# Kernel optimization log

Hardware: AMD Instinct MI355X
Metric: run time of the kernel (lower is better)

Reference implementation:

```python
import jax, jax.numpy as jnp
import numpy as np

N, E, H, L, G = 50000, 500000, 128, 4, 1000
EPS = 1e-7      # GENConv message eps
LN_EPS = 1e-5   # torch LayerNorm default


def setup_inputs() -> dict:
    key = jax.random.key(0)
    ks = jax.random.split(key, 24)
    d = {}
    d["x"] = jax.random.normal(ks[0], (N, 9), jnp.float32)
    d["edge_index"] = jax.random.randint(ks[1], (2, E), 0, N, jnp.int32)
    d["edge_attr"] = jax.random.normal(ks[2], (E, 3), jnp.float32)
    d["batch"] = jnp.sort(jax.random.randint(ks[3], (N,), 0, G, jnp.int32))
    s9, s3, sh, s2h = 1/np.sqrt(9), 1/np.sqrt(3), 1/np.sqrt(H), 1/np.sqrt(2*H)
    u = lambda k, shp, s: jax.random.uniform(k, shp, jnp.float32, -s, s)
    d["enc_node_W"] = u(ks[4], (9, H), s9)
    d["enc_node_b"] = u(ks[5], (H,), s9)
    d["enc_edge_W"] = u(ks[6], (3, H), s3)
    d["enc_edge_b"] = u(ks[7], (H,), s3)
    d["ln_g"] = jnp.ones((L, H), jnp.float32)   # DeepGCNLayer pre-norm affine
    d["ln_b"] = jnp.zeros((L, H), jnp.float32)
    d["W1"] = u(ks[8], (L, H, 2*H), sh)          # GENConv MLP layer 1
    d["b1"] = u(ks[9], (L, 2*H), sh)
    d["mlp_ln_g"] = jnp.ones((L, 2*H), jnp.float32)
    d["mlp_ln_b"] = jnp.zeros((L, 2*H), jnp.float32)
    d["W2"] = u(ks[10], (L, 2*H, H), s2h)        # GENConv MLP layer 2
    d["b2"] = u(ks[11], (L, H), s2h)
    d["t"] = jnp.ones((L,), jnp.float32)         # learnable softmax temperature, init 1.0
    return d


def layernorm(x, g, b):
    mu = x.mean(-1, keepdims=True)
    var = ((x - mu) ** 2).mean(-1, keepdims=True)
    return (x - mu) / jnp.sqrt(var + LN_EPS) * g + b


def genconv(h, src, dst, ea, t, W1, b1, lg, lb, W2, b2):
    # message: relu(x_j + edge_attr) + eps   -> [E, H]
    msg = jax.nn.relu(h[src] + ea) + EPS
    # softmax aggregation over incoming edges, per channel
    logits = t * msg
    m = jax.ops.segment_max(logits, dst, num_segments=N)
    num = jnp.exp(logits - m[dst])
    den = jax.ops.segment_sum(num, dst, num_segments=N)
    alpha = num / den[dst]
    agg = jax.ops.segment_sum(msg * alpha, dst, num_segments=N)
    out = agg + h  # root residual inside GENConv
    z = jax.nn.relu(layernorm(out @ W1 + b1, lg, lb))
    return z @ W2 + b2


def reference(x, edge_index, edge_attr, batch, enc_node_W, enc_node_b,
              enc_edge_W, enc_edge_b, ln_g, ln_b, W1, b1, mlp_ln_g, mlp_ln_b,
              W2, b2, t):
    src, dst = edge_index[0], edge_index[1]
    h = x @ enc_node_W + enc_node_b            # node encoder  [N, H]
    ea = edge_attr @ enc_edge_W + enc_edge_b   # edge encoder  [E, H]
    # layer 0: conv only (DeeperGCN forward uses layers[0].conv directly)
    h = genconv(h, src, dst, ea, t[0], W1[0], b1[0], mlp_ln_g[0], mlp_ln_b[0], W2[0], b2[0])
    # layers 1..L-1: res+ block: x + conv(relu(LN(x))); dropout is identity (eval)
    for i in range(1, L):
        z = jax.nn.relu(layernorm(h, ln_g[i], ln_b[i]))
        h = h + genconv(z, src, dst, ea, t[i], W1[i], b1[i], mlp_ln_g[i], mlp_ln_b[i], W2[i], b2[i])
    h = jax.nn.relu(layernorm(h, ln_g[0], ln_b[0]))  # reuses layer-0 norm
    # global mean pool over graphs
    counts = jax.ops.segment_sum(jnp.ones((N,), h.dtype), batch, num_segments=G)
    sums = jax.ops.segment_sum(h, batch, num_segments=G)
    return sums / jnp.maximum(counts, 1.0)[:, None]
```

## Files before the change

kernel.cpp:

```cpp
#include <hip/hip_runtime.h>

#define NN 50000
#define NE 500000
#define HD 128
#define HD2 256
#define NL 4
#define NG 1000

constexpr float MSG_EPS = 1e-7f;
constexpr float LNEPS   = 1e-5f;

typedef float  f32x4  __attribute__((ext_vector_type(4)));
typedef __bf16 bf16x8 __attribute__((ext_vector_type(8)));

__device__ __forceinline__ unsigned short f2b(float f) {
    unsigned int u = __float_as_uint(f);
    unsigned int r = u + 0x7FFFu + ((u >> 16) & 1u);
    return (unsigned short)(r >> 16);
}
__device__ __forceinline__ float b2f(unsigned short h) {
    return __uint_as_float(((unsigned int)h) << 16);
}
__device__ __forceinline__ unsigned int pack2(float a, float b) {
    return (unsigned int)f2b(a) | ((unsigned int)f2b(b) << 16);
}

#define PREP_BLKS 512
#define ENC_BLKS 25000
#define HIST_BLKS ((NE + 255) / 256)

__global__ void k_setup(const float* __restrict__ x, const float* __restrict__ encW,
                        const float* __restrict__ encB, unsigned short* __restrict__ zb,
                        const float* __restrict__ W1, const float* __restrict__ W2,
                        unsigned short* __restrict__ W1T, unsigned short* __restrict__ W2T,
                        const int* __restrict__ dst, int* __restrict__ counts) {
    int bid = blockIdx.x, tid = threadIdx.x;
    if (bid < PREP_BLKS) {
        int idx = bid * 256 + tid;
        {
            int k = idx & 127, n = (idx >> 7) & 255, l = idx >> 15;
            W1T[idx] = f2b(W1[(l * 128 + k) * 256 + n]);
        }
        {
            int k = idx & 255, n = (idx >> 8) & 127, l = idx >> 15;
            W2T[idx] = f2b(W2[(l * 256 + k) * 128 + n]);
        }
    } else if (bid < PREP_BLKS + ENC_BLKS) {
        int n = (bid - PREP_BLKS) * 2 + (tid >> 7);
        int c = tid & 127;
        float xr[9];
#pragma unroll
        for (int k = 0; k < 9; k++) xr[k] = x[n * 9 + k];
        float acc = encB[c];
#pragma unroll
        for (int k = 0; k < 9; k++) acc = fmaf(xr[k], encW[k * HD + c], acc);
        zb[(size_t)n * HD + c] = f2b(acc);
    } else {
        int e = (bid - PREP_BLKS - ENC_BLKS) * 256 + tid;
        if (e < NE) atomicAdd(&counts[dst[e]], 1);
    }
}

#define SCAN_B 512
#define NSB ((NN + SCAN_B - 1) / SCAN_B)

__global__ void k_scan1(const int* __restrict__ counts, int* __restrict__ incl,
                        int* __restrict__ bsum) {
    __shared__ int s[SCAN_B];
    int i = blockIdx.x * SCAN_B + threadIdx.x;
    int v = (i < NN) ? counts[i] : 0;
    s[threadIdx.x] = v;
    __syncthreads();
    for (int off = 1; off < SCAN_B; off <<= 1) {
        int t = (threadIdx.x >= off) ? s[threadIdx.x - off] : 0;
        __syncthreads();
        s[threadIdx.x] += t;
        __syncthreads();
    }
    if (i < NN) incl[i] = s[threadIdx.x];
    if (threadIdx.x == SCAN_B - 1) bsum[blockIdx.x] = s[threadIdx.x];
}

__global__ void k_scan2(const int* __restrict__ bsum, int* __restrict__ boff, int nb) {
    __shared__ int s[128];
    int v = (threadIdx.x < nb) ? bsum[threadIdx.x] : 0;
    s[threadIdx.x] = v;
    __syncthreads();
    for (int off = 1; off < 128; off <<= 1) {
        int t = (threadIdx.x >= off) ? s[threadIdx.x - off] : 0;
        __syncthreads();
        s[threadIdx.x] += t;
        __syncthreads();
    }
    if (threadIdx.x < nb) boff[threadIdx.x] = s[threadIdx.x] - v;
}

__global__ void k_scan3g(const int* __restrict__ incl, const int* __restrict__ boff,
                         int* __restrict__ row_start, const int* __restrict__ batch,
                         int* __restrict__ gstart) {
    if (blockIdx.x < NSB) {
        int i = blockIdx.x * SCAN_B + threadIdx.x;
        if (i < NN) row_start[i + 1] = incl[i] + boff[blockIdx.x];
        if (i == 0) row_start[0] = 0;
    } else {
        int g = (blockIdx.x - NSB) * SCAN_B + threadIdx.x;
        if (g > NG) return;
        int lo = 0, hi = NN;
        while (lo < hi) {
            int mid = (lo + hi) >> 1;
            if (batch[mid] < g) lo = mid + 1;
            else hi = mid;
        }
        gstart[g] = lo;
    }
}

__global__ void k_scatter(const int* __restrict__ src, const int* __restrict__ dst,
                          const float* __restrict__ eattr, const int* __restrict__ row_start,
                          int* __restrict__ cursor, float4* __restrict__ aperm) {
    int e = blockIdx.x * blockDim.x + threadIdx.x;
    if (e >= NE) return;
    int d = dst[e];
    int p = row_start[d] + atomicAdd(&cursor[d], 1);
    float4 v;
    v.x = eattr[e * 3 + 0];
    v.y = eattr[e * 3 + 1];
    v.z = eattr[e * 3 + 2];
    v.w = __int_as_float(src[e]);
    aperm[p] = v;
}

__device__ __forceinline__ void edge_acc2(float4 a, unsigned int zz, float2 w0, float2 w1,
                                          float2 w2, float2 bb, float tv, float& num0,
                                          float& num1, float& wm0, float& wm1) {
    float zx = b2f((unsigned short)zz), zy = b2f((unsigned short)(zz >> 16));
    float eax = fmaf(a.x, w0.x, fmaf(a.y, w1.x, fmaf(a.z, w2.x, bb.x)));
    float eay = fmaf(a.x, w0.y, fmaf(a.y, w1.y, fmaf(a.z, w2.y, bb.y)));
    float mx = fmaxf(zx + eax, 0.f) + MSG_EPS;
    float my = fmaxf(zy + eay, 0.f) + MSG_EPS;
    float ex = __expf(tv * mx), ey = __expf(tv * my);
    num0 += ex;
    num1 += ey;
    wm0 = fmaf(mx, ex, wm0);
    wm1 = fmaf(my, ey, wm1);
}

__global__ __launch_bounds__(256) void k_aggregate(const unsigned short* __restrict__ zbin,
                                                   const float4* __restrict__ aperm,
                                                   const int* __restrict__ row_start,
                                                   const float* __restrict__ We,
                                                   const float* __restrict__ be,
                                                   const float* __restrict__ t, int layer,
                                                   unsigned int* __restrict__ outb) {
    __shared__ float4 part[4][64];
    int w = threadIdx.x >> 6, lane = threadIdx.x & 63;
    int n = blockIdx.x * 2 + (w >> 1);
    int half = w & 1;
    int c = lane * 2;
    float2 w0 = *(const float2*)&We[c];
    float2 w1 = *(const float2*)&We[HD + c];
    float2 w2 = *(const float2*)&We[2 * HD + c];
    float2 bb = *(const float2*)&be[c];
    float tv = t[layer];
    int s0 = row_start[n], s1 = row_start[n + 1];
    int mid = s0 + ((s1 - s0 + 1) >> 1);
    int lo = half ? mid : s0;
    int hi = half ? s1 : mid;
    float num0 = 0.f, num1 = 0.f, wm0 = 0.f, wm1 = 0.f;
    const unsigned int* z32 = (const unsigned int*)zbin;
    int p = lo;
    for (; p + 4 <= hi; p += 4) {
        float4 A[4];
#pragma unroll
        for (int j = 0; j < 4; j++) A[j] = aperm[p + j];
        unsigned int Z[4];
#pragma unroll
        for (int j = 0; j < 4; j++) {
            int sj = __builtin_amdgcn_readfirstlane(__float_as_int(A[j].w));
            Z[j] = z32[(size_t)sj * 64 + lane];
        }
#pragma unroll
        for (int j = 0; j < 4; j++)
            edge_acc2(A[j], Z[j], w0, w1, w2, bb, tv, num0, num1, wm0, wm1);
    }
    for (; p < hi; p++) {
        float4 a = aperm[p];
        int sj = __builtin_amdgcn_readfirstlane(__float_as_int(a.w));
        unsigned int zz = z32[(size_t)sj * 64 + lane];
        edge_acc2(a, zz, w0, w1, w2, bb, tv, num0, num1, wm0, wm1);
    }
    part[w][lane] = make_float4(num0, num1, wm0, wm1);
    __syncthreads();
    if (half == 0) {
        float4 a = part[w][lane];
        float4 b = part[w + 1][lane];
        float n0 = a.x + b.x, n1 = a.y + b.y;
        float m0 = a.z + b.z, m1 = a.w + b.w;
        unsigned int zn = z32[(size_t)n * 64 + lane];
        bool has = s1 > s0;
        float ox = (has ? (m0 / n0) : 0.f) + b2f((unsigned short)zn);
        float oy = (has ? (m1 / n1) : 0.f) + b2f((unsigned short)(zn >> 16));
        outb[(size_t)n * 64 + lane] = pack2(ox, oy);
    }
}

#define BM 32
#define HS_LD 264
#define HT_LD 136

__global__ __launch_bounds__(256) void k_mlp(const unsigned short* __restrict__ outb,
                                             const unsigned short* __restrict__ W1T,
                                             const float* __restrict__ b1l,
                                             const float* __restrict__ lgl,
                                             const float* __restrict__ lbl,
                                             const unsigned short* __restrict__ W2T,
                                             const float* __restrict__ b2l,
                                             unsigned short* __restrict__ h,
                                             const float* __restrict__ gn,
                                             const float* __restrict__ bn,
                                             unsigned short* __restrict__ zb,
                                             int add_residual) {
    __shared__ __align__(16) unsigned short Hs[BM * HS_LD];
    __shared__ __align__(16) unsigned short Ht[BM * HT_LD];
    __shared__ __align__(16) float2 st1[2][16][4];

    int nb = blockIdx.x * BM;
    int tid = threadIdx.x;
    int w = tid >> 6, lane = tid & 63, q = lane >> 4, i = lane & 15;

    f32x4 acc[2][4];
#pragma unroll
    for (int rt = 0; rt < 2; rt++)
#pragma unroll
        for (int ct = 0; ct < 4; ct++) acc[rt][ct] = (f32x4){0.f, 0.f, 0.f, 0.f};

    bf16x8 acur[2], bcur[4];
#pragma unroll
    for (int rt = 0; rt < 2; rt++) {
        int row = nb + rt * 16 + i;
        acur[rt] = (row < NN) ? *(const bf16x8*)&outb[(size_t)row * HD + q * 8]
                              : (bf16x8)(__bf16)0.f;
    }
#pragma unroll
    for (int ct = 0; ct < 4; ct++)
        bcur[ct] = *(const bf16x8*)&W1T[(w * 64 + ct * 16 + i) * HD + q * 8];

#pragma unroll
    for (int ks = 0; ks < 4; ks++) {
        bf16x8 anxt[2], bnxt[4];
        if (ks < 3) {
#pragma unroll
            for (int rt = 0; rt < 2; rt++) {
                int row = nb + rt * 16 + i;
                anxt[rt] = (row < NN)
                               ? *(const bf16x8*)&outb[(size_t)row * HD + (ks + 1) * 32 + q * 8]
                               : (bf16x8)(__bf16)0.f;
            }
#pragma unroll
            for (int ct = 0; ct < 4; ct++)
                bnxt[ct] =
                    *(const bf16x8*)&W1T[(w * 64 + ct * 16 + i) * HD + (ks + 1) * 32 + q * 8];
        }
#pragma unroll
        for (int rt = 0; rt < 2; rt++)
#pragma unroll
            for (int ct = 0; ct < 4; ct++)
                acc[rt][ct] =
                    __builtin_amdgcn_mfma_f32_16x16x32_bf16(acur[rt], bcur[ct], acc[rt][ct],
                                                            0, 0, 0);
        if (ks < 3) {
#pragma unroll
            for (int rt = 0; rt < 2; rt++) acur[rt] = anxt[rt];
#pragma unroll
            for (int ct = 0; ct < 4; ct++) bcur[ct] = bnxt[ct];
        }
    }

#pragma unroll
    for (int ct = 0; ct < 4; ct++) {
        float bb = b1l[w * 64 + ct * 16 + i];
#pragma unroll
        for (int rt = 0; rt < 2; rt++)
#pragma unroll
            for (int r = 0; r < 4; r++) acc[rt][ct][r] += bb;
    }

    {
        float sv[2][4], qv[2][4];
#pragma unroll
        for (int rt = 0; rt < 2; rt++)
#pragma unroll
            for (int r = 0; r < 4; r++) {
                float s = acc[rt][0][r] + acc[rt][1][r] + acc[rt][2][r] + acc[rt][3][r];
                float sq = 0.f;
#pragma unroll
                for (int ct = 0; ct < 4; ct++) sq = fmaf(acc[rt][ct][r], acc[rt][ct][r], sq);
                sv[rt][r] = s;
                qv[rt][r] = sq;
            }
#pragma unroll
        for (int m = 1; m <= 8; m <<= 1)
#pragma unroll
            for (int rt = 0; rt < 2; rt++)
#pragma unroll
                for (int r = 0; r < 4; r++) {
                    sv[rt][r] += __shfl_xor(sv[rt][r], m);
                    qv[rt][r] += __shfl_xor(qv[rt][r], m);
                }
        if (i == 0) {
#pragma unroll
            for (int rt = 0; rt < 2; rt++)
#pragma unroll
                for (int r = 0; r < 4; r++)
                    st1[rt][q * 4 + r][w] = make_float2(sv[rt][r], qv[rt][r]);
        }
    }
    __syncthreads();

    {
        float mu[2][4], inv[2][4];
#pragma unroll
        for (int rt = 0; rt < 2; rt++)
#pragma unroll
            for (int r = 0; r < 4; r++) {
                const float4* sp = (const float4*)&st1[rt][q * 4 + r][0];
                float4 a = sp[0], b = sp[1];
                float S = a.x + a.z + b.x + b.z;
                float Q = a.y + a.w + b.y + b.w;
                float m_ = S * (1.f / 256.f);
                float v_ = Q * (1.f / 256.f) - m_ * m_;
                mu[rt][r] = m_;
                inv[rt][r] = rsqrtf(v_ + LNEPS);
            }
#pragma unroll
        for (int ct = 0; ct < 4; ct++) {
            float g = lgl[w * 64 + ct * 16 + i];
            float c = lbl[w * 64 + ct * 16 + i];
#pragma unroll
            for (int rt = 0; rt < 2; rt++)
#pragma unroll
                for (int r = 0; r < 4; r++) {
                    float v =
                        fmaxf(fmaf((acc[rt][ct][r] - mu[rt][r]) * inv[rt][r], g, c), 0.f);
                    Hs[(rt * 16 + q * 4 + r) * HS_LD + w * 64 + ct * 16 + i] = f2b(v);
                }
        }
    }
    __syncthreads();

    f32x4 acc2[2][2];
#pragma unroll
    for (int rt = 0; rt < 2; rt++)
#pragma unroll
        for (int ct = 0; ct < 2; ct++) acc2[rt][ct] = (f32x4){0.f, 0.f, 0.f, 0.f};

    bf16x8 hc[2], bc[2];
#pragma unroll
    for (int rt = 0; rt < 2; rt++) hc[rt] = *(const bf16x8*)&Hs[(rt * 16 + i) * HS_LD + q * 8];
#pragma unroll
    for (int ct = 0; ct < 2; ct++)
        bc[ct] = *(const bf16x8*)&W2T[(w * 32 + ct * 16 + i) * HD2 + q * 8];

#pragma unroll
    for (int ks = 0; ks < 8; ks++) {
        bf16x8 hn[2], bn2[2];
        if (ks < 7) {
#pragma unroll
            for (int rt = 0; rt < 2; rt++)
                hn[rt] = *(const bf16x8*)&Hs[(rt * 16 + i) * HS_LD + (ks + 1) * 32 + q * 8];
#pragma unroll
            for (int ct = 0; ct < 2; ct++)
                bn2[ct] =
                    *(const bf16x8*)&W2T[(w * 32 + ct * 16 + i) * HD2 + (ks + 1) * 32 + q * 8];
        }
#pragma unroll
        for (int rt = 0; rt < 2; rt++)
#pragma unroll
            for (int ct = 0; ct < 2; ct++)
                acc2[rt][ct] = __builtin_amdgcn_mfma_f32_16x16x32_bf16(hc[rt], bc[ct],
                                                                      acc2[rt][ct], 0, 0, 0);
        if (ks < 7) {
#pragma unroll
            for (int rt = 0; rt < 2; rt++) hc[rt] = hn[rt];
#pragma unroll
            for (int ct = 0; ct < 2; ct++) bc[ct] = bn2[ct];
        }
    }

#pragma unroll
    for (int ct = 0; ct < 2; ct++) {
        float bb = b2l[w * 32 + ct * 16 + i];
#pragma unroll
        for (int rt = 0; rt < 2; rt++)
#pragma unroll
            for (int r = 0; r < 4; r++)
                Ht[(rt * 16 + q * 4 + r) * HT_LD + w * 32 + ct * 16 + i] =
                    f2b(acc2[rt][ct][r] + bb);
    }
    __syncthreads();

    {
        const unsigned int* Ht32 = (const unsigned int*)Ht;
        unsigned int* h32 = (unsigned int*)h;
        unsigned int* zb32 = (unsigned int*)zb;
        float2 gg = *(const float2*)&gn[lane * 2];
        float2 cc = *(const float2*)&bn[lane * 2];
        for (int rr = w; rr < BM; rr += 4) {
            int row = nb + rr;
            if (row >= NN) break;
            unsigned int tv = Ht32[rr * (HT_LD / 2) + lane];
            float cx = b2f((unsigned short)tv), cy = b2f((unsigned short)(tv >> 16));
            if (add_residual) {
                unsigned int hv = h32[(size_t)row * 64 + lane];
                cx += b2f((unsigned short)hv);
                cy += b2f((unsigned short)(hv >> 16));
            }
            h32[(size_t)row * 64 + lane] = pack2(cx, cy);
            float s = cx + cy, sq = cx * cx + cy * cy;
#pragma unroll
            for (int m = 32; m >= 1; m >>= 1) {
                s += __shfl_xor(s, m);
                sq += __shfl_xor(sq, m);
            }
            float mu = s * (1.f / 128.f);
            float var = sq * (1.f / 128.f) - mu * mu;
            float inv = rsqrtf(var + LNEPS);
            float z0 = fmaxf(fmaf((cx - mu) * inv, gg.x, cc.x), 0.f);
            float z1 = fmaxf(fmaf((cy - mu) * inv, gg.y, cc.y), 0.f);
            zb32[(size_t)row * 64 + lane] = pack2(z0, z1);
        }
    }
}

__global__ void k_pool(const unsigned short* __restrict__ zb, const int* __restrict__ gstart,
                       float* __restrict__ out) {
    int g = blockIdx.x;
    int c = threadIdx.x;
    int a = gstart[g], b = gstart[g + 1];
    float s0 = 0.f, s1 = 0.f;
    int n = a;
    for (; n + 2 <= b; n += 2) {
        s0 += b2f(zb[(size_t)n * HD + c]);
        s1 += b2f(zb[(size_t)(n + 1) * HD + c]);
    }
    if (n < b) s0 += b2f(zb[(size_t)n * HD + c]);
    out[g * HD + c] = (s0 + s1) / fmaxf((float)(b - a), 1.f);
}

extern "C" void kernel_launch(void* const* d_in, const int* in_sizes, int n_in, void* d_out,
                              int out_size, void* d_ws, size_t ws_size, hipStream_t stream) {
    const float* x     = (const float*)d_in[0];
    const int* ei      = (const int*)d_in[1];
    const float* eattr = (const float*)d_in[2];
    const int* batch   = (const int*)d_in[3];
    const float* encW  = (const float*)d_in[4];
    const float* encB  = (const float*)d_in[5];
    const float* eW    = (const float*)d_in[6];
    const float* eB    = (const float*)d_in[7];
    const float* ln_g  = (const float*)d_in[8];
    const float* ln_b  = (const float*)d_in[9];
    const float* W1    = (const float*)d_in[10];
    const float* b1    = (const float*)d_in[11];
    const float* mlg   = (const float*)d_in[12];
    const float* mlb   = (const float*)d_in[13];
    const float* W2    = (const float*)d_in[14];
    const float* b2    = (const float*)d_in[15];
    const float* t     = (const float*)d_in[16];
    const int* src = ei;
    const int* dst = ei + NE;

    char* w = (char*)d_ws;
    auto alloc = [&](size_t bytes) {
        char* p = w;
        w += (bytes + 255) & ~size_t(255);
        return p;
    };
    unsigned short* h    = (unsigned short*)alloc(sizeof(unsigned short) * NN * HD);
    unsigned short* zb   = (unsigned short*)alloc(sizeof(unsigned short) * NN * HD);
    unsigned int* outb   = (unsigned int*)alloc(sizeof(unsigned int) * NN * HD / 2);
    float4* aperm        = (float4*)alloc(sizeof(float4) * NE);
    int* row_start       = (int*)alloc(sizeof(int) * (NN + 1));
    int* counts          = (int*)alloc(sizeof(int) * NN);
    int* cursor          = (int*)alloc(sizeof(int) * NN);
    int* incl            = (int*)alloc(sizeof(int) * NN);
    int* bsum            = (int*)alloc(sizeof(int) * 128);
    int* boff            = (int*)alloc(sizeof(int) * 128);
    int* gstart          = (int*)alloc(sizeof(int) * (NG + 1));
    unsigned short* W1T  = (unsigned short*)alloc(sizeof(unsigned short) * NL * HD * HD2);
    unsigned short* W2T  = (unsigned short*)alloc(sizeof(unsigned short) * NL * HD2 * HD);

    hipMemsetAsync(counts, 0, sizeof(int) * NN, stream);
    hipMemsetAsync(cursor, 0, sizeof(int) * NN, stream);

    k_setup<<<PREP_BLKS + ENC_BLKS + HIST_BLKS, 256, 0, stream>>>(x, encW, encB, zb, W1, W2,
                                                                  W1T, W2T, dst, counts);
    k_scan1<<<NSB, SCAN_B, 0, stream>>>(counts, incl, bsum);
    k_scan2<<<1, 128, 0, stream>>>(bsum, boff, NSB);
    k_scan3g<<<NSB + 2, SCAN_B, 0, stream>>>(incl, boff, row_start, batch, gstart);
    k_scatter<<<(NE + 255) / 256, 256, 0, stream>>>(src, dst, eattr, row_start, cursor, aperm);

    for (int l = 0; l < NL; l++) {
        k_aggregate<<<NN / 2, 256, 0, stream>>>(zb, aperm, row_start, eW, eB, t, l, outb);
        int ln_next = (l + 1) % NL;
        k_mlp<<<(NN + BM - 1) / BM, 256, 0, stream>>>(
            (const unsigned short*)outb, W1T + (size_t)l * HD * HD2, b1 + l * HD2,
            mlg + l * HD2, mlb + l * HD2, W2T + (size_t)l * HD2 * HD, b2 + l * HD, h,
            ln_g + ln_next * HD, ln_b + ln_next * HD, zb, l > 0);
    }
    k_pool<<<NG, HD, 0, stream>>>(zb, gstart, (float*)d_out);
}
```

Baseline: 547.0 us.

## Assign one wavefront per node in aggregation and vectorise edge math

```diff
diff --git a/kernel.cpp b/kernel.cpp
--- a/kernel.cpp
+++ b/kernel.cpp
@@ -11,6 +11,7 @@
 constexpr float LNEPS   = 1e-5f;
 
 typedef float  f32x4  __attribute__((ext_vector_type(4)));
+typedef float  f32x2  __attribute__((ext_vector_type(2)));
 typedef __bf16 bf16x8 __attribute__((ext_vector_type(8)));
 
 __device__ __forceinline__ unsigned short f2b(float f) {
@@ -130,19 +131,21 @@
     aperm[p] = v;
 }
 
-__device__ __forceinline__ void edge_acc2(float4 a, unsigned int zz, float2 w0, float2 w1,
-                                          float2 w2, float2 bb, float tv, float& num0,
-                                          float& num1, float& wm0, float& wm1) {
-    float zx = b2f((unsigned short)zz), zy = b2f((unsigned short)(zz >> 16));
-    float eax = fmaf(a.x, w0.x, fmaf(a.y, w1.x, fmaf(a.z, w2.x, bb.x)));
-    float eay = fmaf(a.x, w0.y, fmaf(a.y, w1.y, fmaf(a.z, w2.y, bb.y)));
-    float mx = fmaxf(zx + eax, 0.f) + MSG_EPS;
-    float my = fmaxf(zy + eay, 0.f) + MSG_EPS;
-    float ex = __expf(tv * mx), ey = __expf(tv * my);
-    num0 += ex;
-    num1 += ey;
-    wm0 = fmaf(mx, ex, wm0);
-    wm1 = fmaf(my, ey, wm1);
+__device__ __forceinline__ void edge_acc2(float4 a, unsigned int zz, f32x2 w0, f32x2 w1,
+                                          f32x2 w2, f32x2 bb, float tv, f32x2& num,
+                                          f32x2& wm) {
+    f32x2 z;
+    z.x = b2f((unsigned short)zz);
+    z.y = b2f((unsigned short)(zz >> 16));
+    f32x2 m = z + bb + a.x * w0 + a.y * w1 + a.z * w2;
+    m.x = fmaxf(m.x, 0.f);
+    m.y = fmaxf(m.y, 0.f);
+    f32x2 tm = tv * m;
+    f32x2 e;
+    e.x = __expf(tm.x);
+    e.y = __expf(tm.y);
+    num += e;
+    wm += m * e;
 }
 
 __global__ __launch_bounds__(256) void k_aggregate(const unsigned short* __restrict__ zbin,
@@ -152,24 +155,33 @@
                                                    const float* __restrict__ be,
                                                    const float* __restrict__ t, int layer,
                                                    unsigned int* __restrict__ outb) {
-    __shared__ float4 part[4][64];
     int w = threadIdx.x >> 6, lane = threadIdx.x & 63;
-    int n = blockIdx.x * 2 + (w >> 1);
-    int half = w & 1;
+    int n = blockIdx.x * 4 + w;
+    if (n >= NN) return;
     int c = lane * 2;
-    float2 w0 = *(const float2*)&We[c];
-    float2 w1 = *(const float2*)&We[HD + c];
-    float2 w2 = *(const float2*)&We[2 * HD + c];
-    float2 bb = *(const float2*)&be[c];
+    f32x2 w0 = *(const f32x2*)&We[c];
+    f32x2 w1 = *(const f32x2*)&We[HD + c];
+    f32x2 w2 = *(const f32x2*)&We[2 * HD + c];
+    f32x2 bb = *(const f32x2*)&be[c];
     float tv = t[layer];
     int s0 = row_start[n], s1 = row_start[n + 1];
-    int mid = s0 + ((s1 - s0 + 1) >> 1);
-    int lo = half ? mid : s0;
-    int hi = half ? s1 : mid;
-    float num0 = 0.f, num1 = 0.f, wm0 = 0.f, wm1 = 0.f;
+    f32x2 num = (f32x2){0.f, 0.f}, wm = (f32x2){0.f, 0.f};
     const unsigned int* z32 = (const unsigned int*)zbin;
-    int p = lo;
-    for (; p + 4 <= hi; p += 4) {
+    int p = s0;
+    for (; p + 8 <= s1; p += 8) {
+        float4 A[8];
+#pragma unroll
+        for (int j = 0; j < 8; j++) A[j] = aperm[p + j];
+        unsigned int Z[8];
+#pragma unroll
+        for (int j = 0; j < 8; j++) {
+            int sj = __builtin_amdgcn_readfirstlane(__float_as_int(A[j].w));
+            Z[j] = z32[(size_t)sj * 64 + lane];
+        }
+#pragma unroll
+        for (int j = 0; j < 8; j++) edge_acc2(A[j], Z[j], w0, w1, w2, bb, tv, num, wm);
+    }
+    for (; p + 4 <= s1; p += 4) {
         float4 A[4];
 #pragma unroll
         for (int j = 0; j < 4; j++) A[j] = aperm[p + j];
@@ -180,28 +192,19 @@
             Z[j] = z32[(size_t)sj * 64 + lane];
         }
 #pragma unroll
-        for (int j = 0; j < 4; j++)
-            edge_acc2(A[j], Z[j], w0, w1, w2, bb, tv, num0, num1, wm0, wm1);
-    }
-    for (; p < hi; p++) {
+        for (int j = 0; j < 4; j++) edge_acc2(A[j], Z[j], w0, w1, w2, bb, tv, num, wm);
+    }
+    for (; p < s1; p++) {
         float4 a = aperm[p];
         int sj = __builtin_amdgcn_readfirstlane(__float_as_int(a.w));
         unsigned int zz = z32[(size_t)sj * 64 + lane];
-        edge_acc2(a, zz, w0, w1, w2, bb, tv, num0, num1, wm0, wm1);
-    }
-    part[w][lane] = make_float4(num0, num1, wm0, wm1);
-    __syncthreads();
-    if (half == 0) {
-        float4 a = part[w][lane];
-        float4 b = part[w + 1][lane];
-        float n0 = a.x + b.x, n1 = a.y + b.y;
-        float m0 = a.z + b.z, m1 = a.w + b.w;
-        unsigned int zn = z32[(size_t)n * 64 + lane];
-        bool has = s1 > s0;
-        float ox = (has ? (m0 / n0) : 0.f) + b2f((unsigned short)zn);
-        float oy = (has ? (m1 / n1) : 0.f) + b2f((unsigned short)(zn >> 16));
-        outb[(size_t)n * 64 + lane] = pack2(ox, oy);
-    }
+        edge_acc2(a, zz, w0, w1, w2, bb, tv, num, wm);
+    }
+    unsigned int zn = z32[(size_t)n * 64 + lane];
+    bool has = s1 > s0;
+    float ox = (has ? (wm.x / num.x + MSG_EPS) : 0.f) + b2f((unsigned short)zn);
+    float oy = (has ? (wm.y / num.y + MSG_EPS) : 0.f) + b2f((unsigned short)(zn >> 16));
+    outb[(size_t)n * 64 + lane] = pack2(ox, oy);
 }
 
 #define BM 32
@@ -500,7 +503,7 @@
     k_scatter<<<(NE + 255) / 256, 256, 0, stream>>>(src, dst, eattr, row_start, cursor, aperm);
 
     for (int l = 0; l < NL; l++) {
-        k_aggregate<<<NN / 2, 256, 0, stream>>>(zb, aperm, row_start, eW, eB, t, l, outb);
+        k_aggregate<<<(NN + 3) / 4, 256, 0, stream>>>(zb, aperm, row_start, eW, eB, t, l, outb);
         int ln_next = (l + 1) % NL;
         k_mlp<<<(NN + BM - 1) / BM, 256, 0, stream>>>(
             (const unsigned short*)outb, W1T + (size_t)l * HD * HD2, b1 + l * HD2,
```

After: 509.1 us. 6.9% less time.
